# Kernel optimization log

Hardware: AMD Instinct MI355X
Metric: run time of the kernel (lower is better)

The kernel has to match this reference:

```python
import jax, jax.numpy as jnp
import numpy as np
from jax import lax

N_ITER = 100          # max_iter=100 in forward's sparse_fit call
EPS = 1e-8            # multiplicative-update denominator guard
H_IMG, W_IMG = 1024, 1024
R2 = 4                # self.r = r*2 with default r=2


def setup_inputs() -> dict:
    key = jax.random.key(0)
    k1, k2, k3, k4, k5 = jax.random.split(key, 5)
    N = H_IMG * W_IMG
    pic = jax.random.uniform(k1, (3, H_IMG, W_IMG), jnp.float32)            # source RGB image in [0,1]
    W_target = jax.random.uniform(k2, (3, R2), jnp.float32, 0.05, 1.0)      # target stain matrix (nmft.H)
    Ht_RM = jax.random.uniform(k3, (), jnp.float32, 0.5, 2.0)               # 0.99-quantile of target concentrations
    W0 = jax.random.uniform(k4, (N, R2), jnp.float32, 0.05, 1.0)            # NMF concentration init (torchnmf W)
    H0 = jax.random.uniform(k5, (3, R2), jnp.float32, 0.05, 1.0)            # NMF stain-matrix init (torchnmf H)
    return {"pic": pic, "W_target": W_target, "Ht_RM": Ht_RM, "W0": W0, "H0": H0}


def _nmf_fit(V, H0, W0):
    # V (3,N) ~= Hd @ Wc.T ; Hd (3,r) stain matrix, Wc (N,r) concentrations.
    # Standard beta=2 (Frobenius) multiplicative updates, N_ITER iterations.
    def step(carry, _):
        Hd, Wc = carry
        Wc = Wc * (V.T @ Hd) / (Wc @ (Hd.T @ Hd) + EPS)   # (N,r): skinny GEMMs via r x r Gram
        Hd = Hd * (V @ Wc) / (Hd @ (Wc.T @ Wc) + EPS)     # (3,r)
        return (Hd, Wc), None

    (Hd, Wc), _ = lax.scan(jax.checkpoint(step), (H0, W0), None, length=N_ITER)
    return Hd, Wc


def reference(pic, W_target, Ht_RM, W0, H0):
    c, h, w = pic.shape
    V = -jnp.log(jnp.clip(pic.reshape(3, -1), 0.01, 0.99))   # optical density, (3,N)
    Hd, Wc = _nmf_fit(V, H0, W0)
    H_s = Wc.T                                               # (r,N) source concentrations
    H_sn = H_s * Ht_RM / jnp.quantile(H_s, 0.99)             # quantile normalization to target
    out = jnp.exp(-(W_target @ H_sn)).reshape(c, h, w)       # recompose with target stains
    return jnp.clip(out, 0.0, 1.0)
```

## Files before the change

kernel.cpp:

```cpp
#include <hip/hip_runtime.h>
#include <math.h>


#define N_PIX (1024*1024)
#define NB    256
#define BS    512
#define NWAVE (BS/64)
#define TT    (NB*BS)
#define PPT   (N_PIX/TT)
#define NIT   100
#define EPSI  1e-8f
#define NBINS 2048
#define NGRP  16
#define TSTR  24

#define OFF_GH0_B 0
#define OFF_GH1_B 8192
#define OFF_T1_B  16384
#define OFF_T2_B  (16384 + NB*2*TSTR*8)
#define WS_BYTES  (OFF_T2_B + NGRP*2*TSTR*8)

typedef unsigned long long u64;

__device__ __forceinline__ u64 ld_tag(const u64* p) {
    return __hip_atomic_load(p, __ATOMIC_RELAXED, __HIP_MEMORY_SCOPE_AGENT);
}
__device__ __forceinline__ void st_tag(u64* p, u64 v) {
    __hip_atomic_store(p, v, __ATOMIC_RELAXED, __HIP_MEMORY_SCOPE_AGENT);
}
__device__ __forceinline__ unsigned ld_rlx_u(const unsigned* p) {
    return __hip_atomic_load(p, __ATOMIC_RELAXED, __HIP_MEMORY_SCOPE_AGENT);
}
__device__ __forceinline__ u64 pack_tag(unsigned ep, float x) {
    return ((u64)ep << 32) | (u64)__float_as_uint(x);
}
__device__ __forceinline__ float spin_val(const u64* p, unsigned ep) {
    const u64 thr = ((u64)ep) << 32;
    u64 v = ld_tag(p);
    while (v < thr) { __builtin_amdgcn_s_sleep(1); v = ld_tag(p); }
    return __uint_as_float((unsigned)v);
}
__device__ __forceinline__ void spin_only(const u64* p, unsigned ep) {
    const u64 thr = ((u64)ep) << 32;
    while (ld_tag(p) < thr) __builtin_amdgcn_s_sleep(1);
}

__global__ __launch_bounds__(BS)
void he_norm_kernel(const float* __restrict__ pic,
                    const float* __restrict__ Wt,
                    const float* __restrict__ HtRM,
                    const float* __restrict__ W0,
                    const float* __restrict__ H0,
                    float* __restrict__ out,
                    unsigned char* __restrict__ ws)
{
    const int tid  = threadIdx.x;
    const int blk  = blockIdx.x;
    const int g    = blk*BS + tid;
    const int wave = tid >> 6;
    const int lane = tid & 63;
    const int grp  = blk >> 4;
    const int isLeader = ((blk & 15) == 0);
    const int grpBase  = grp << 4;

    unsigned* gh0 = (unsigned*)(ws + OFF_GH0_B);
    unsigned* gh1 = (unsigned*)(ws + OFF_GH1_B);
    u64*      T1  = (u64*)(ws + OFF_T1_B);
    u64*      T2  = (u64*)(ws + OFF_T2_B);

    __shared__ float sAcc[BS*23];
    __shared__ float sPr[16][22];
    __shared__ float sS[22], sHd[12], sG[16], sWt[12], sScal[2];
    __shared__ float sRed[NWAVE][2];
    __shared__ unsigned sHist[NBINS];
    __shared__ unsigned sSeg[256];
    __shared__ int      sBstar;
    __shared__ unsigned sCumB;

    if (tid < 12) { sHd[tid] = H0[tid]; sWt[tid] = Wt[tid]; }
    __syncthreads();
    if (tid < 16) {
        int s_ = tid >> 2, r_ = tid & 3;
        sG[tid] = sHd[s_]*sHd[r_] + sHd[4+s_]*sHd[4+r_] + sHd[8+s_]*sHd[8+r_];
    }

    float v0[PPT], v1[PPT], v2[PPT];
    float w[PPT][4];
    #pragma unroll
    for (int k = 0; k < PPT; k++) {
        int i = g + k*TT;
        float4 wv = ((const float4*)W0)[i];
        w[k][0]=wv.x; w[k][1]=wv.y; w[k][2]=wv.z; w[k][3]=wv.w;
        v0[k] = -logf(fminf(fmaxf(pic[i],           0.01f), 0.99f));
        v1[k] = -logf(fminf(fmaxf(pic[N_PIX  + i],  0.01f), 0.99f));
        v2[k] = -logf(fminf(fmaxf(pic[2*N_PIX + i], 0.01f), 0.99f));
    }
    __syncthreads();

    for (int t = 0; t < NIT; ++t) {
        float hd[12], gg[16];
        #pragma unroll
        for (int j = 0; j < 12; j++) hd[j] = sHd[j];
        #pragma unroll
        for (int j = 0; j < 16; j++) gg[j] = sG[j];

        float acc[22];
        #pragma unroll
        for (int j = 0; j < 22; j++) acc[j] = 0.f;

        #pragma unroll
        for (int k = 0; k < PPT; k++) {
            float wn[4];
            #pragma unroll
            for (int r = 0; r < 4; r++) {
                float num = v0[k]*hd[r] + v1[k]*hd[4+r] + v2[k]*hd[8+r];
                float den = w[k][0]*gg[r] + w[k][1]*gg[4+r]
                          + w[k][2]*gg[8+r] + w[k][3]*gg[12+r] + EPSI;
                float rc = __builtin_amdgcn_rcpf(den);
                rc = rc * (2.0f - den*rc);
                wn[r] = w[k][r] * num * rc;
            }
            #pragma unroll
            for (int r = 0; r < 4; r++) {
                acc[r]    += v0[k]*wn[r];
                acc[4+r]  += v1[k]*wn[r];
                acc[8+r]  += v2[k]*wn[r];
            }
            acc[12]+=wn[0]*wn[0]; acc[13]+=wn[0]*wn[1]; acc[14]+=wn[0]*wn[2]; acc[15]+=wn[0]*wn[3];
            acc[16]+=wn[1]*wn[1]; acc[17]+=wn[1]*wn[2]; acc[18]+=wn[1]*wn[3];
            acc[19]+=wn[2]*wn[2]; acc[20]+=wn[2]*wn[3]; acc[21]+=wn[3]*wn[3];
            w[k][0]=wn[0]; w[k][1]=wn[1]; w[k][2]=wn[2]; w[k][3]=wn[3];
        }

        if (t == NIT-1) break;
        const unsigned ep  = (unsigned)(t + 1);
        const int      par = (int)(ep & 1u);

        #pragma unroll
        for (int j = 0; j < 22; j++) sAcc[tid*23 + j] = acc[j];
        __syncthreads();
        if (tid < 352) {
            int seg = tid / 22, j = tid - seg*22;
            const float* row = &sAcc[(seg*32)*23 + j];
            float p0=0.f, p1=0.f, p2=0.f, p3=0.f;
            #pragma unroll
            for (int b = 0; b < 32; b += 4) {
                p0 += row[(b+0)*23]; p1 += row[(b+1)*23];
                p2 += row[(b+2)*23]; p3 += row[(b+3)*23];
            }
            sPr[seg][j] = (p0+p1)+(p2+p3);
        }
        __syncthreads();
        if (tid < 22) {
            float bp = 0.f;
            #pragma unroll
            for (int sg = 0; sg < 16; sg++) bp += sPr[sg][tid];
            st_tag(&T1[(blk*2 + par)*TSTR + tid], pack_tag(ep, bp));
        }
        __syncthreads();

        if (isLeader) {
            if (tid < 352) {
                int m = tid / 22, j = tid - m*22;
                sPr[m][j] = spin_val(&T1[((grpBase + m)*2 + par)*TSTR + j], ep);
            }
            __syncthreads();
            if (tid < 22) {
                float gp = 0.f;
                #pragma unroll
                for (int m = 0; m < 16; m++) gp += sPr[m][tid];
                st_tag(&T2[(grp*2 + par)*TSTR + tid], pack_tag(ep, gp));
            }
            __syncthreads();
        }

        if (tid < 352) {
            int g2 = tid / 22, j = tid - g2*22;
            sPr[g2][j] = spin_val(&T2[(g2*2 + par)*TSTR + j], ep);
        }
        __syncthreads();
        if (tid < 22) {
            float s = 0.f;
            #pragma unroll
            for (int g2 = 0; g2 < 16; g2++) s += sPr[g2][tid];
            sS[tid] = s;
        }
        __syncthreads();

        if (wave == 0) {
            if (lane < 12) {
                int c = lane >> 2, r = lane & 3;
                const int base[4] = {12, 16, 19, 21};
                float den = EPSI;
                #pragma unroll
                for (int s2 = 0; s2 < 4; s2++) {
                    int lo = (s2 < r) ? s2 : r, hi = (s2 < r) ? r : s2;
                    den += sHd[c*4 + s2] * sS[base[lo] + (hi - lo)];
                }
                float nhd = sHd[lane] * sS[lane] / den;
                sHd[lane] = nhd;
            }
            if (lane < 16) {
                int s_ = lane >> 2, r_ = lane & 3;
                sG[lane] = sHd[s_]*sHd[r_] + sHd[4+s_]*sHd[4+r_] + sHd[8+s_]*sHd[8+r_];
            }
        }
        __syncthreads();
    }

    {
        float m = 0.f;
        #pragma unroll
        for (int k = 0; k < PPT; k++)
            #pragma unroll
            for (int r = 0; r < 4; r++) m = fmaxf(m, w[k][r]);
        #pragma unroll
        for (int off = 32; off > 0; off >>= 1) m = fmaxf(m, __shfl_down(m, off, 64));
        if (lane == 0) sRed[wave][0] = m;
        __syncthreads();
        if (tid == 0) {
            float mm = 0.f;
            for (int wv2 = 0; wv2 < NWAVE; wv2++) mm = fmaxf(mm, sRed[wv2][0]);
            st_tag(&T1[(blk*2 + 0)*TSTR + 0], pack_tag(100u, mm));
        }
        if (tid < NB) sAcc[tid] = spin_val(&T1[(tid*2 + 0)*TSTR + 0], 100u);
        __syncthreads();
        if (tid < NB) {
            float mv = sAcc[tid];
            #pragma unroll
            for (int off = 32; off > 0; off >>= 1) mv = fmaxf(mv, __shfl_down(mv, off, 64));
            if (lane == 0) sRed[wave][1] = mv;
        }
        __syncthreads();
        if (tid == 0) {
            float mm = 0.f;
            for (int wv2 = 0; wv2 < 4; wv2++) mm = fmaxf(mm, sRed[wv2][1]);
            sScal[0] = mm * 1.0000002f;
        }
        __syncthreads();
    }
    const float gmax   = sScal[0];
    const float scale0 = (float)NBINS / gmax;

    for (int i = tid; i < NBINS; i += BS) sHist[i] = 0u;
    __syncthreads();
    #pragma unroll
    for (int k = 0; k < PPT; k++)
        #pragma unroll
        for (int r = 0; r < 4; r++) {
            int b = (int)(w[k][r] * scale0);
            b = min(b, NBINS - 1);
            atomicAdd(&sHist[b], 1u);
        }
    __syncthreads();
    for (int i = tid; i < NBINS; i += BS) if (sHist[i]) atomicAdd(&gh0[i], sHist[i]);
    __builtin_amdgcn_s_waitcnt(0);
    __syncthreads();
    if (tid == 0) st_tag(&T1[(blk*2 + 1)*TSTR + 0], pack_tag(101u, 0.f));
    if (tid < NB) spin_only(&T1[(tid*2 + 1)*TSTR + 0], 101u);
    __syncthreads();

    const double kfd = 0.99 * (double)(4*N_PIX - 1);
    if (tid < 256) {
        unsigned s2 = 0;
        for (int i = 0; i < 8; i++) s2 += ld_rlx_u(&gh0[tid*8 + i]);
        sSeg[tid] = s2;
    }
    __syncthreads();
    if (tid == 0) {
        unsigned cum = 0; int seg = 0;
        for (int i2 = 0; i2 < 256; i2++) {
            if ((double)(cum + sSeg[i2]) > kfd) { seg = i2; break; }
            cum += sSeg[i2];
        }
        unsigned c2 = cum; int b = seg*8;
        for (int i2 = 0; i2 < 8; i2++) {
            unsigned h = ld_rlx_u(&gh0[seg*8 + i2]);
            if ((double)(c2 + h) > kfd) { b = seg*8 + i2; break; }
            c2 += h;
        }
        sBstar = b; sCumB = c2;
    }
    __syncthreads();
    const int   bstar  = sBstar;
    const float lo1    = (float)bstar / scale0;
    const float scale1 = scale0 * (float)NBINS;

    for (int i = tid; i < NBINS; i += BS) sHist[i] = 0u;
    __syncthreads();
    #pragma unroll
    for (int k = 0; k < PPT; k++)
        #pragma unroll
        for (int r = 0; r < 4; r++) {
            int b0 = min((int)(w[k][r] * scale0), NBINS - 1);
            if (b0 == bstar) {
                int b1 = (int)((w[k][r] - lo1) * scale1);
                b1 = max(0, min(b1, NBINS - 1));
                atomicAdd(&sHist[b1], 1u);
            }
        }
    __syncthreads();
    for (int i = tid; i < NBINS; i += BS) if (sHist[i]) atomicAdd(&gh1[i], sHist[i]);
    __builtin_amdgcn_s_waitcnt(0);
    __syncthreads();
    if (tid == 0) st_tag(&T1[(blk*2 + 0)*TSTR + 0], pack_tag(102u, 0.f));
    if (tid < NB) spin_only(&T1[(tid*2 + 0)*TSTR + 0], 102u);
    __syncthreads();

    if (tid < 256) {
        unsigned s2 = 0;
        for (int i = 0; i < 8; i++) s2 += ld_rlx_u(&gh1[tid*8 + i]);
        sSeg[tid] = s2;
    }
    __syncthreads();
    if (tid == 0) {
        double jf = kfd - (double)sCumB;
        unsigned cum = 0; int seg = 0;
        for (int i2 = 0; i2 < 256; i2++) {
            if ((double)(cum + sSeg[i2]) > jf) { seg = i2; break; }
            cum += sSeg[i2];
        }
        unsigned c3 = cum; int bb = seg*8; unsigned hh = 1;
        for (int i2 = 0; i2 < 8; i2++) {
            unsigned h = ld_rlx_u(&gh1[seg*8 + i2]);
            if ((double)(c3 + h) > jf) { bb = seg*8 + i2; hh = h; break; }
            c3 += h;
        }
        double frac = (jf - (double)c3 + 0.5) / (double)hh;
        frac = fmin(fmax(frac, 0.0), 1.0);
        double q = (double)lo1 + ((double)bb + frac) / (double)scale1;
        sScal[1] = (float)((double)HtRM[0] / q);
    }
    __syncthreads();
    const float sc = sScal[1];

    #pragma unroll
    for (int k = 0; k < PPT; k++) {
        int i = g + k*TT;
        #pragma unroll
        for (int c = 0; c < 3; c++) {
            float d = sWt[c*4+0]*w[k][0] + sWt[c*4+1]*w[k][1]
                    + sWt[c*4+2]*w[k][2] + sWt[c*4+3]*w[k][3];
            float e = expf(-d * sc);
            out[c*N_PIX + i] = fminf(fmaxf(e, 0.f), 1.f);
        }
    }
}

extern "C" void kernel_launch(void* const* d_in, const int* in_sizes, int n_in,
                              void* d_out, int out_size, void* d_ws, size_t ws_size,
                              hipStream_t stream) {
    const float* pic  = (const float*)d_in[0];
    const float* Wt   = (const float*)d_in[1];
    const float* HtRM = (const float*)d_in[2];
    const float* W0   = (const float*)d_in[3];
    const float* H0   = (const float*)d_in[4];
    float* out = (float*)d_out;

    hipMemsetAsync(d_ws, 0, WS_BYTES, stream);
    he_norm_kernel<<<dim3(NB), dim3(BS), 0, stream>>>(
        pic, Wt, HtRM, W0, H0, out, (unsigned char*)d_ws);
}
```

Baseline: 580.4 us.

## Replace leader-based grid reduction with 2D all-to-all butterfly and register-resident H

The two-level grid reduction, where group leaders gathered 16 block partials and every block then waited on the leaders, is replaced by a symmetric two-stage exchange. Each block sums its row of 16 blocks, publishes that row sum, then sums the matching column of row sums, so no block waits for a leader. The stain matrix and Gram matrix are kept in registers and updated redundantly by every wave, which removes several __syncthreads and the shared-memory round trip. Spin loops drop s_sleep and the accumulator stride is padded so stores can be vectorised. The cost is more global polling traffic from all 256 blocks, a larger T2 workspace, and redundant H-update arithmetic in every wave.

```diff
diff --git a/kernel.cpp b/kernel.cpp
--- a/kernel.cpp
+++ b/kernel.cpp
@@ -11,14 +11,14 @@
 #define NIT   100
 #define EPSI  1e-8f
 #define NBINS 2048
-#define NGRP  16
 #define TSTR  24
+#define SSTR  24
 
 #define OFF_GH0_B 0
 #define OFF_GH1_B 8192
 #define OFF_T1_B  16384
 #define OFF_T2_B  (16384 + NB*2*TSTR*8)
-#define WS_BYTES  (OFF_T2_B + NGRP*2*TSTR*8)
+#define WS_BYTES  (OFF_T2_B + NB*2*TSTR*8)
 
 typedef unsigned long long u64;
 
@@ -33,6 +33,12 @@
 }
 __device__ __forceinline__ u64 pack_tag(unsigned ep, float x) {
     return ((u64)ep << 32) | (u64)__float_as_uint(x);
+}
+__device__ __forceinline__ float spin_fast(const u64* p, unsigned ep) {
+    const u64 thr = ((u64)ep) << 32;
+    u64 v = ld_tag(p);
+    while (v < thr) v = ld_tag(p);
+    return __uint_as_float((unsigned)v);
 }
 __device__ __forceinline__ float spin_val(const u64* p, unsigned ep) {
     const u64 thr = ((u64)ep) << 32;
@@ -59,29 +65,33 @@
     const int g    = blk*BS + tid;
     const int wave = tid >> 6;
     const int lane = tid & 63;
-    const int grp  = blk >> 4;
-    const int isLeader = ((blk & 15) == 0);
-    const int grpBase  = grp << 4;
+    const int rowB = blk & ~15;
+    const int col  = blk & 15;
 
     unsigned* gh0 = (unsigned*)(ws + OFF_GH0_B);
     unsigned* gh1 = (unsigned*)(ws + OFF_GH1_B);
     u64*      T1  = (u64*)(ws + OFF_T1_B);
     u64*      T2  = (u64*)(ws + OFF_T2_B);
 
-    __shared__ float sAcc[BS*23];
-    __shared__ float sPr[16][22];
-    __shared__ float sS[22], sHd[12], sG[16], sWt[12], sScal[2];
+    __shared__ float sAcc[BS*SSTR];
+    __shared__ float sPrA[16][22];
+    __shared__ float sPrB[16][22];
+    __shared__ float sWv[NWAVE*32];
+    __shared__ float sWt[12], sScal[2];
     __shared__ float sRed[NWAVE][2];
     __shared__ unsigned sHist[NBINS];
     __shared__ unsigned sSeg[256];
     __shared__ int      sBstar;
     __shared__ unsigned sCumB;
 
-    if (tid < 12) { sHd[tid] = H0[tid]; sWt[tid] = Wt[tid]; }
-    __syncthreads();
-    if (tid < 16) {
-        int s_ = tid >> 2, r_ = tid & 3;
-        sG[tid] = sHd[s_]*sHd[r_] + sHd[4+s_]*sHd[4+r_] + sHd[8+s_]*sHd[8+r_];
+    if (tid < 12) sWt[tid] = Wt[tid];
+    float hd[12], gg[16];
+    #pragma unroll
+    for (int j = 0; j < 12; j++) hd[j] = H0[j];
+    #pragma unroll
+    for (int j = 0; j < 16; j++) {
+        int s_ = j >> 2, r_ = j & 3;
+        gg[j] = hd[s_]*hd[r_] + hd[4+s_]*hd[4+r_] + hd[8+s_]*hd[8+r_];
     }
 
     float v0[PPT], v1[PPT], v2[PPT];
@@ -98,12 +108,6 @@
     __syncthreads();
 
     for (int t = 0; t < NIT; ++t) {
-        float hd[12], gg[16];
-        #pragma unroll
-        for (int j = 0; j < 12; j++) hd[j] = sHd[j];
-        #pragma unroll
-        for (int j = 0; j < 16; j++) gg[j] = sG[j];
-
         float acc[22];
         #pragma unroll
         for (int j = 0; j < 22; j++) acc[j] = 0.f;
@@ -136,76 +140,94 @@
         const unsigned ep  = (unsigned)(t + 1);
         const int      par = (int)(ep & 1u);
 
-        #pragma unroll
-        for (int j = 0; j < 22; j++) sAcc[tid*23 + j] = acc[j];
+        {
+            float4* dst = (float4*)&sAcc[tid*SSTR];
+            dst[0] = make_float4(acc[0], acc[1], acc[2], acc[3]);
+            dst[1] = make_float4(acc[4], acc[5], acc[6], acc[7]);
+            dst[2] = make_float4(acc[8], acc[9], acc[10], acc[11]);
+            dst[3] = make_float4(acc[12], acc[13], acc[14], acc[15]);
+            dst[4] = make_float4(acc[16], acc[17], acc[18], acc[19]);
+            *((float2*)&sAcc[tid*SSTR + 20]) = make_float2(acc[20], acc[21]);
+        }
         __syncthreads();
         if (tid < 352) {
             int seg = tid / 22, j = tid - seg*22;
-            const float* row = &sAcc[(seg*32)*23 + j];
+            const float* row = &sAcc[(seg*32)*SSTR + j];
             float p0=0.f, p1=0.f, p2=0.f, p3=0.f;
             #pragma unroll
             for (int b = 0; b < 32; b += 4) {
-                p0 += row[(b+0)*23]; p1 += row[(b+1)*23];
-                p2 += row[(b+2)*23]; p3 += row[(b+3)*23];
-            }
-            sPr[seg][j] = (p0+p1)+(p2+p3);
+                p0 += row[(b+0)*SSTR]; p1 += row[(b+1)*SSTR];
+                p2 += row[(b+2)*SSTR]; p3 += row[(b+3)*SSTR];
+            }
+            sPrA[seg][j] = (p0+p1)+(p2+p3);
         }
         __syncthreads();
         if (tid < 22) {
             float bp = 0.f;
             #pragma unroll
-            for (int sg = 0; sg < 16; sg++) bp += sPr[sg][tid];
+            for (int sg = 0; sg < 16; sg++) bp += sPrA[sg][tid];
             st_tag(&T1[(blk*2 + par)*TSTR + tid], pack_tag(ep, bp));
         }
-        __syncthreads();
-
-        if (isLeader) {
-            if (tid < 352) {
-                int m = tid / 22, j = tid - m*22;
-                sPr[m][j] = spin_val(&T1[((grpBase + m)*2 + par)*TSTR + j], ep);
-            }
-            __syncthreads();
-            if (tid < 22) {
-                float gp = 0.f;
+
+        if (tid < 352) {
+            int m = tid / 22, j = tid - m*22;
+            sPrB[m][j] = spin_fast(&T1[((rowB + m)*2 + par)*TSTR + j], ep);
+        }
+        __syncthreads();
+        if (tid < 22) {
+            float rs = 0.f;
+            #pragma unroll
+            for (int m = 0; m < 16; m++) rs += sPrB[m][tid];
+            st_tag(&T2[(blk*2 + par)*TSTR + tid], pack_tag(ep, rs));
+        }
+
+        if (tid < 352) {
+            int m = tid / 22, j = tid - m*22;
+            sPrA[m][j] = spin_fast(&T2[((m*16 + col)*2 + par)*TSTR + j], ep);
+        }
+        __syncthreads();
+
+        {
+            if (lane < 22) {
+                float s = 0.f;
                 #pragma unroll
-                for (int m = 0; m < 16; m++) gp += sPr[m][tid];
-                st_tag(&T2[(grp*2 + par)*TSTR + tid], pack_tag(ep, gp));
-            }
-            __syncthreads();
-        }
-
-        if (tid < 352) {
-            int g2 = tid / 22, j = tid - g2*22;
-            sPr[g2][j] = spin_val(&T2[(g2*2 + par)*TSTR + j], ep);
-        }
-        __syncthreads();
-        if (tid < 22) {
-            float s = 0.f;
-            #pragma unroll
-            for (int g2 = 0; g2 < 16; g2++) s += sPr[g2][tid];
-            sS[tid] = s;
-        }
-        __syncthreads();
-
-        if (wave == 0) {
-            if (lane < 12) {
-                int c = lane >> 2, r = lane & 3;
-                const int base[4] = {12, 16, 19, 21};
-                float den = EPSI;
+                for (int m = 0; m < 16; m++) s += sPrA[m][lane];
+                sWv[wave*32 + lane] = s;
+            }
+            float ss[22];
+            {
+                const float4* wr = (const float4*)&sWv[wave*32];
+                float4 a0 = wr[0], a1 = wr[1], a2 = wr[2], a3 = wr[3], a4 = wr[4];
+                float2 a5 = ((const float2*)&sWv[wave*32])[10];
+                ss[0]=a0.x; ss[1]=a0.y; ss[2]=a0.z; ss[3]=a0.w;
+                ss[4]=a1.x; ss[5]=a1.y; ss[6]=a1.z; ss[7]=a1.w;
+                ss[8]=a2.x; ss[9]=a2.y; ss[10]=a2.z; ss[11]=a2.w;
+                ss[12]=a3.x; ss[13]=a3.y; ss[14]=a3.z; ss[15]=a3.w;
+                ss[16]=a4.x; ss[17]=a4.y; ss[18]=a4.z; ss[19]=a4.w;
+                ss[20]=a5.x; ss[21]=a5.y;
+            }
+            float nhd[12];
+            const int base[4] = {12, 16, 19, 21};
+            #pragma unroll
+            for (int c = 0; c < 3; c++)
                 #pragma unroll
-                for (int s2 = 0; s2 < 4; s2++) {
-                    int lo = (s2 < r) ? s2 : r, hi = (s2 < r) ? r : s2;
-                    den += sHd[c*4 + s2] * sS[base[lo] + (hi - lo)];
+                for (int r = 0; r < 4; r++) {
+                    float den = EPSI;
+                    #pragma unroll
+                    for (int s2 = 0; s2 < 4; s2++) {
+                        int lo = (s2 < r) ? s2 : r, hi = (s2 < r) ? r : s2;
+                        den += hd[c*4 + s2] * ss[base[lo] + (hi - lo)];
+                    }
+                    nhd[c*4+r] = hd[c*4+r] * ss[c*4+r] / den;
                 }
-                float nhd = sHd[lane] * sS[lane] / den;
-                sHd[lane] = nhd;
-            }
-            if (lane < 16) {
-                int s_ = lane >> 2, r_ = lane & 3;
-                sG[lane] = sHd[s_]*sHd[r_] + sHd[4+s_]*sHd[4+r_] + sHd[8+s_]*sHd[8+r_];
-            }
-        }
-        __syncthreads();
+            #pragma unroll
+            for (int j = 0; j < 12; j++) hd[j] = nhd[j];
+            #pragma unroll
+            for (int j = 0; j < 16; j++) {
+                int s_ = j >> 2, r_ = j & 3;
+                gg[j] = hd[s_]*hd[r_] + hd[4+s_]*hd[4+r_] + hd[8+s_]*hd[8+r_];
+            }
+        }
     }
 
     {
```

After: 661.8 us. +14.0%, slower.
